# Kernel optimization log

Measured on AMD Instinct MI355X. Metric: run time of the kernel, lower is better.

## Reference

```python
import jax, jax.numpy as jnp
import numpy as np

B, C, KC, H, W = 8, 256, 32, 128, 128


def setup_inputs() -> dict:
    key = jax.random.key(0)
    ks = jax.random.split(key, 5)
    x = jax.random.normal(ks[0], (B, C, H, W), dtype=jnp.float32)
    Wq = jax.random.normal(ks[1], (KC, C), dtype=jnp.float32) / np.sqrt(C)
    Wk = jax.random.normal(ks[2], (KC, C), dtype=jnp.float32) / np.sqrt(C)
    Wv = jax.random.normal(ks[3], (C, C), dtype=jnp.float32) / np.sqrt(C)
    bq = jnp.zeros((KC,), dtype=jnp.float32)
    bk = jnp.zeros((KC,), dtype=jnp.float32)
    bv = jnp.zeros((C,), dtype=jnp.float32)
    gamma = jax.random.uniform(ks[4], (1,), dtype=jnp.float32)
    return {"x": x, "Wq": Wq, "bq": bq, "Wk": Wk, "bk": bk, "Wv": Wv, "bv": bv, "gamma": gamma}


def reference(x, Wq, bq, Wk, bk, Wv, bv, gamma):
    b, c, h, w = x.shape
    n = h * w
    xf = x.reshape(b, c, n)  # [B,C,N]
    # 1x1 convs == per-pixel linear maps
    q = jnp.einsum('kc,bcn->bkn', Wq, xf) + bq[None, :, None]
    k = jnp.einsum('kc,bcn->bkn', Wk, xf) + bk[None, :, None]
    v = jnp.einsum('vc,bcn->bvn', Wv, xf) + bv[None, :, None]
    fm = lambda t: jax.nn.elu(t) + 1.0  # elu+1 feature map
    qm = fm(q)  # [B,KC,N]
    km = fm(k)  # [B,KC,N]
    kv = jnp.einsum('bkn,bvn->bkv', km, v)          # kv context [B,KC,C]
    z = km.sum(axis=-1)                              # z norm factor [B,KC]
    qkv = jnp.einsum('bkn,bkv->bnv', qm, kv)        # [B,N,C]
    qz = jnp.einsum('bkn,bk->bn', qm, z)            # [B,N]
    normed = qkv / jnp.maximum(qz, 1e-6)[..., None]  # [B,N,C]
    out = normed.transpose(0, 2, 1).reshape(b, c, h, w)
    return gamma[0] * out + x
```

## Files before the change

### kernel.cpp

```cpp
#include <hip/hip_runtime.h>

#define Bn  8
#define Cn  256
#define KCn 32
#define Nn  16384

typedef __attribute__((ext_vector_type(8))) short bf16x8;
typedef __attribute__((ext_vector_type(4))) short short4v;
typedef __attribute__((ext_vector_type(4))) float f32x4;

__device__ __forceinline__ float elup1(float v) {
    return v > 0.0f ? v + 1.0f : __expf(v);
}
__device__ __forceinline__ short f2bf(float f) {
    unsigned u = __float_as_uint(f);
    return (short)((u + 0x7FFFu + ((u >> 16) & 1u)) >> 16);
}

__global__ __launch_bounds__(512, 4) void k_km_S(const float* __restrict__ x,
                                                 const float* __restrict__ Wk,
                                                 const float* __restrict__ bk,
                                                 float* __restrict__ S,
                                                 float* __restrict__ Z) {
    __shared__ short xs[256][40];
    __shared__ short wks[32][264];
    __shared__ short kml[32][264];
    __shared__ float bkl[KCn];

    const int t = threadIdx.x;
    const int b = blockIdx.y;
    const int n0 = blockIdx.x * 256;
    const int lane = t & 63, wv = t >> 6;
    const int g = lane >> 4, l15 = lane & 15;
    const int pxw = wv * 32;
    const float* xb = x + (size_t)b * Cn * Nn;

    {
        const int row = t >> 4, col0 = (t & 15) * 16;
        const float* src = Wk + row * Cn + col0;
        bf16x8 v0, v1;
#pragma unroll
        for (int i = 0; i < 8; ++i) { v0[i] = f2bf(src[i]); v1[i] = f2bf(src[8 + i]); }
        *(bf16x8*)&wks[row][col0] = v0;
        *(bf16x8*)&wks[row][col0 + 8] = v1;
        if (t < KCn) bkl[t] = bk[t];
    }

    f32x4 acc1[2][2] = {};
    for (int kc = 0; kc < 8; ++kc) {
        if (kc) __syncthreads();
        {
            const int px = t & 255, ch = t >> 8;
            const float* sp = xb + (size_t)(kc * 32 + ch * 16) * Nn + n0 + px;
            bf16x8 v0, v1;
#pragma unroll
            for (int i = 0; i < 8; ++i) v0[i] = f2bf(sp[(size_t)i * Nn]);
#pragma unroll
            for (int i = 0; i < 8; ++i) v1[i] = f2bf(sp[(size_t)(8 + i) * Nn]);
            *(bf16x8*)&xs[px][ch * 16] = v0;
            *(bf16x8*)&xs[px][ch * 16 + 8] = v1;
        }
        __syncthreads();
        const bf16x8 af0 = *(const bf16x8*)&wks[l15][kc * 32 + g * 8];
        const bf16x8 af1 = *(const bf16x8*)&wks[16 + l15][kc * 32 + g * 8];
        const bf16x8 bf0 = *(const bf16x8*)&xs[pxw + l15][g * 8];
        const bf16x8 bf1 = *(const bf16x8*)&xs[pxw + 16 + l15][g * 8];
        acc1[0][0] = __builtin_amdgcn_mfma_f32_16x16x32_bf16(af0, bf0, acc1[0][0], 0, 0, 0);
        acc1[0][1] = __builtin_amdgcn_mfma_f32_16x16x32_bf16(af0, bf1, acc1[0][1], 0, 0, 0);
        acc1[1][0] = __builtin_amdgcn_mfma_f32_16x16x32_bf16(af1, bf0, acc1[1][0], 0, 0, 0);
        acc1[1][1] = __builtin_amdgcn_mfma_f32_16x16x32_bf16(af1, bf1, acc1[1][1], 0, 0, 0);
    }

    {
        float zp[2][4] = {{0.f,0.f,0.f,0.f},{0.f,0.f,0.f,0.f}};
#pragma unroll
        for (int mt = 0; mt < 2; ++mt)
#pragma unroll
            for (int j = 0; j < 4; ++j) {
                const int kf = mt * 16 + g * 4 + j;
                const float bkv = bkl[kf];
#pragma unroll
                for (int nt = 0; nt < 2; ++nt) {
                    const float v = elup1(acc1[mt][nt][j] + bkv);
                    zp[mt][j] += v;
                    kml[kf][pxw + nt * 16 + l15] = f2bf(v);
                }
            }
#pragma unroll
        for (int mt = 0; mt < 2; ++mt)
#pragma unroll
            for (int j = 0; j < 4; ++j) {
                float s = zp[mt][j];
                s += __shfl_xor(s, 1); s += __shfl_xor(s, 2);
                s += __shfl_xor(s, 4); s += __shfl_xor(s, 8);
                if (l15 == 0) atomicAdd(&Z[b * KCn + mt * 16 + g * 4 + j], s);
            }
    }
    __syncthreads();

    f32x4 acc2[2][2] = {};
    const int crow = wv * 32;
    for (int ks = 0; ks < 8; ++ks) {
        bf16x8 a2[2];
#pragma unroll
        for (int mt = 0; mt < 2; ++mt) {
            const float* ap = xb + (size_t)(crow + mt * 16 + l15) * Nn + n0 + ks * 32 + g * 8;
            const float4 f0 = *(const float4*)ap;
            const float4 f1 = *(const float4*)(ap + 4);
            bf16x8 v;
            v[0] = f2bf(f0.x); v[1] = f2bf(f0.y); v[2] = f2bf(f0.z); v[3] = f2bf(f0.w);
            v[4] = f2bf(f1.x); v[5] = f2bf(f1.y); v[6] = f2bf(f1.z); v[7] = f2bf(f1.w);
            a2[mt] = v;
        }
        const bf16x8 b20 = *(const bf16x8*)&kml[l15][ks * 32 + g * 8];
        const bf16x8 b21 = *(const bf16x8*)&kml[16 + l15][ks * 32 + g * 8];
        acc2[0][0] = __builtin_amdgcn_mfma_f32_16x16x32_bf16(a2[0], b20, acc2[0][0], 0, 0, 0);
        acc2[0][1] = __builtin_amdgcn_mfma_f32_16x16x32_bf16(a2[0], b21, acc2[0][1], 0, 0, 0);
        acc2[1][0] = __builtin_amdgcn_mfma_f32_16x16x32_bf16(a2[1], b20, acc2[1][0], 0, 0, 0);
        acc2[1][1] = __builtin_amdgcn_mfma_f32_16x16x32_bf16(a2[1], b21, acc2[1][1], 0, 0, 0);
    }
    float* Sb = S + (size_t)b * Cn * KCn;
#pragma unroll
    for (int mt = 0; mt < 2; ++mt)
#pragma unroll
        for (int nt = 0; nt < 2; ++nt)
#pragma unroll
            for (int j = 0; j < 4; ++j)
                atomicAdd(&Sb[(crow + mt * 16 + g * 4 + j) * KCn + nt * 16 + l15],
                          acc2[mt][nt][j]);
}

__global__ __launch_bounds__(256) void k_kv(const float* __restrict__ Wv,
                                            const float* __restrict__ bv,
                                            const float* __restrict__ S,
                                            const float* __restrict__ Z,
                                            unsigned short* __restrict__ KVT) {
    __shared__ float Sl[Cn][KCn];
    __shared__ float zl[KCn];
    const int t = threadIdx.x;
    const int b = blockIdx.y;
    const int vc0 = blockIdx.x * 32;
    const float* Sb = S + (size_t)b * Cn * KCn;
#pragma unroll
    for (int i = 0; i < 32; ++i) ((float*)Sl)[i * 256 + t] = Sb[i * 256 + t];
    if (t < KCn) zl[t] = Z[b * KCn + t];
    __syncthreads();
    const int vc = vc0 + (t >> 3);
    const int kq = (t & 7) * 4;
    const float bvv = bv[vc];
    f32x4 acc;
#pragma unroll
    for (int i = 0; i < 4; ++i) acc[i] = bvv * zl[kq + i];
    const float* wv = Wv + (size_t)vc * Cn;
#pragma unroll 4
    for (int c = 0; c < Cn; ++c) {
        const float w = wv[c];
        const f32x4 s4 = *(const f32x4*)&Sl[c][kq];
#pragma unroll
        for (int i = 0; i < 4; ++i) acc[i] += w * s4[i];
    }
    unsigned short* kp = KVT + ((size_t)b * Cn + vc) * KCn + kq;
    ushort4 o;
    o.x = (unsigned short)f2bf(acc[0]); o.y = (unsigned short)f2bf(acc[1]);
    o.z = (unsigned short)f2bf(acc[2]); o.w = (unsigned short)f2bf(acc[3]);
    *(ushort4*)kp = o;
}

__global__ __launch_bounds__(512, 4) void k_out(const float* __restrict__ x,
                                                const float* __restrict__ Wq,
                                                const float* __restrict__ bq,
                                                const unsigned short* __restrict__ KVT,
                                                const float* __restrict__ Z,
                                                const float* __restrict__ gamma,
                                                float* __restrict__ out) {
    __shared__ short xs[256][40];
    __shared__ short wqs[32][264];
    __shared__ short qml[256][40];
    __shared__ short kvtl[272][40];
    __shared__ float bql[KCn];

    const int t = threadIdx.x;
    const int b = blockIdx.y;
    const int n0 = blockIdx.x * 256;
    const int lane = t & 63, wv = t >> 6;
    const int g = lane >> 4, l15 = lane & 15;
    const int pxw = wv * 32;
    const float* xb = x + (size_t)b * Cn * Nn;

    {
        const int row = t >> 4, col0 = (t & 15) * 16;
        const float* src = Wq + row * Cn + col0;
        bf16x8 v0, v1;
#pragma unroll
        for (int i = 0; i < 8; ++i) { v0[i] = f2bf(src[i]); v1[i] = f2bf(src[8 + i]); }
        *(bf16x8*)&wqs[row][col0] = v0;
        *(bf16x8*)&wqs[row][col0 + 8] = v1;
        if (t < KCn) bql[t] = bq[t];
        const int vc = t >> 1, half = t & 1;
        const bf16x8* kvsrc =
            (const bf16x8*)(KVT + (size_t)b * Cn * KCn + vc * KCn + half * 16);
        *(bf16x8*)&kvtl[vc][half * 16]     = kvsrc[0];
        *(bf16x8*)&kvtl[vc][half * 16 + 8] = kvsrc[1];
        if (t < KCn) kvtl[256][t] = f2bf(Z[b * KCn + t]);
        for (int i = t; i < 15 * 40; i += 512) kvtl[257 + i / 40][i % 40] = 0;
    }

    f32x4 acc1[2][2] = {};
    for (int kc = 0; kc < 8; ++kc) {
        if (kc) __syncthreads();
        {
            const int px = t & 255, ch = t >> 8;
            const float* sp = xb + (size_t)(kc * 32 + ch * 16) * Nn + n0 + px;
            bf16x8 v0, v1;
#pragma unroll
            for (int i = 0; i < 8; ++i) v0[i] = f2bf(sp[(size_t)i * Nn]);
#pragma unroll
            for (int i = 0; i < 8; ++i) v1[i] = f2bf(sp[(size_t)(8 + i) * Nn]);
            *(bf16x8*)&xs[px][ch * 16] = v0;
            *(bf16x8*)&xs[px][ch * 16 + 8] = v1;
        }
        __syncthreads();
        const bf16x8 af0 = *(const bf16x8*)&wqs[l15][kc * 32 + g * 8];
        const bf16x8 af1 = *(const bf16x8*)&wqs[16 + l15][kc * 32 + g * 8];
        const bf16x8 bf0 = *(const bf16x8*)&xs[pxw + l15][g * 8];
        const bf16x8 bf1 = *(const bf16x8*)&xs[pxw + 16 + l15][g * 8];
        acc1[0][0] = __builtin_amdgcn_mfma_f32_16x16x32_bf16(af0, bf0, acc1[0][0], 0, 0, 0);
        acc1[0][1] = __builtin_amdgcn_mfma_f32_16x16x32_bf16(af0, bf1, acc1[0][1], 0, 0, 0);
        acc1[1][0] = __builtin_amdgcn_mfma_f32_16x16x32_bf16(af1, bf0, acc1[1][0], 0, 0, 0);
        acc1[1][1] = __builtin_amdgcn_mfma_f32_16x16x32_bf16(af1, bf1, acc1[1][1], 0, 0, 0);
    }

#pragma unroll
    for (int mt = 0; mt < 2; ++mt)
#pragma unroll
        for (int nt = 0; nt < 2; ++nt) {
            short4v q4;
#pragma unroll
            for (int j = 0; j < 4; ++j)
                q4[j] = f2bf(elup1(acc1[mt][nt][j] + bql[mt * 16 + g * 4 + j]));
            *(short4v*)&qml[pxw + nt * 16 + l15][mt * 16 + g * 4] = q4;
        }

    const bf16x8 qb0 = *(const bf16x8*)&qml[pxw + l15][g * 8];
    const bf16x8 qb1 = *(const bf16x8*)&qml[pxw + 16 + l15][g * 8];
    f32x4 u0 = {}, u1 = {};
    {
        const bf16x8 az = *(const bf16x8*)&kvtl[256 + l15][g * 8];
        u0 = __builtin_amdgcn_mfma_f32_16x16x32_bf16(az, qb0, u0, 0, 0, 0);
        u1 = __builtin_amdgcn_mfma_f32_16x16x32_bf16(az, qb1, u1, 0, 0, 0);
    }
    const float qz0 = __shfl(u0[0], l15);
    const float qz1 = __shfl(u1[0], l15);
    const float gm = gamma[0];
    const float r0 = gm / fmaxf(qz0, 1e-6f);
    const float r1 = gm / fmaxf(qz1, 1e-6f);
    float* ob = out + (size_t)b * Cn * Nn + n0;
    const float* xrb = xb + n0;
    const int p0 = pxw + l15, p1 = pxw + 16 + l15;
#pragma unroll 4
    for (int mt = 0; mt < 16; ++mt) {
        const bf16x8 a = *(const bf16x8*)&kvtl[mt * 16 + l15][g * 8];
        f32x4 c0 = {}, c1 = {};
        c0 = __builtin_amdgcn_mfma_f32_16x16x32_bf16(a, qb0, c0, 0, 0, 0);
        c1 = __builtin_amdgcn_mfma_f32_16x16x32_bf16(a, qb1, c1, 0, 0, 0);
#pragma unroll
        for (int j = 0; j < 4; ++j) {
            const size_t ro = (size_t)(mt * 16 + g * 4 + j) * Nn;
            ob[ro + p0] = c0[j] * r0 + xrb[ro + p0];
            ob[ro + p1] = c1[j] * r1 + xrb[ro + p1];
        }
    }
}

extern "C" void kernel_launch(void* const* d_in, const int* in_sizes, int n_in,
                              void* d_out, int out_size, void* d_ws, size_t ws_size,
                              hipStream_t stream) {
    const float* x     = (const float*)d_in[0];
    const float* Wq    = (const float*)d_in[1];
    const float* bq    = (const float*)d_in[2];
    const float* Wk    = (const float*)d_in[3];
    const float* bk    = (const float*)d_in[4];
    const float* Wv    = (const float*)d_in[5];
    const float* bv    = (const float*)d_in[6];
    const float* gamma = (const float*)d_in[7];
    float* out = (float*)d_out;

    float* S = (float*)d_ws;
    float* Z = S + (size_t)Bn * Cn * KCn;
    unsigned short* KVT = (unsigned short*)(Z + (size_t)Bn * KCn);

    hipMemsetAsync(d_ws, 0, ((size_t)Bn * Cn * KCn + Bn * KCn) * sizeof(float), stream);
    k_km_S<<<dim3(64, Bn), 512, 0, stream>>>(x, Wk, bk, S, Z);
    k_kv  <<<dim3(8, Bn), 256, 0, stream>>>(Wv, bv, S, Z, KVT);
    k_out <<<dim3(64, Bn), 512, 0, stream>>>(x, Wq, bq, KVT, Z, gamma, out);
}
```

Before: 394.4 us.

## Halve pixel tile, pre-convert weights to bf16, and register-prefetch x loads

Adds a tiny prep kernel that converts Wk and Wq to bf16 once, so the main kernels stop converting the weights per block into shared memory and read them directly from global. Both heavy kernels now use 128-pixel tiles with twice as many blocks, smaller shared memory footprints and higher occupancy bounds. The x tile for the next channel chunk is prefetched into registers while the current MFMA step runs. k_out reuses the x staging buffer for the q features. The trade-off is an extra launch, double-counted block setup, more Z atomics, and uncached global weight fragment loads per wave.

```diff
diff --git a/kernel.cpp b/kernel.cpp
--- a/kernel.cpp
+++ b/kernel.cpp
@@ -17,90 +17,79 @@
     return (short)((u + 0x7FFFu + ((u >> 16) & 1u)) >> 16);
 }
 
-__global__ __launch_bounds__(512, 4) void k_km_S(const float* __restrict__ x,
-                                                 const float* __restrict__ Wk,
+__global__ void k_prep(const float* __restrict__ Wk, const float* __restrict__ Wq,
+                       unsigned short* __restrict__ Wkbf, unsigned short* __restrict__ Wqbf) {
+    const int i = blockIdx.x * 512 + threadIdx.x;
+    Wkbf[i] = (unsigned short)f2bf(Wk[i]);
+    Wqbf[i] = (unsigned short)f2bf(Wq[i]);
+}
+
+__global__ __launch_bounds__(512, 8) void k_km_S(const float* __restrict__ x,
+                                                 const unsigned short* __restrict__ Wkbf,
                                                  const float* __restrict__ bk,
                                                  float* __restrict__ S,
                                                  float* __restrict__ Z) {
-    __shared__ short xs[256][40];
-    __shared__ short wks[32][264];
-    __shared__ short kml[32][264];
+    __shared__ short xs[128][40];
+    __shared__ short kml[32][136];
     __shared__ float bkl[KCn];
 
-    const int t = threadIdx.x;
-    const int b = blockIdx.y;
-    const int n0 = blockIdx.x * 256;
+    const int t = threadIdx.x, b = blockIdx.y, n0 = blockIdx.x * 128;
     const int lane = t & 63, wv = t >> 6;
     const int g = lane >> 4, l15 = lane & 15;
-    const int pxw = wv * 32;
+    const int pxw = wv * 16;
     const float* xb = x + (size_t)b * Cn * Nn;
-
-    {
-        const int row = t >> 4, col0 = (t & 15) * 16;
-        const float* src = Wk + row * Cn + col0;
-        bf16x8 v0, v1;
-#pragma unroll
-        for (int i = 0; i < 8; ++i) { v0[i] = f2bf(src[i]); v1[i] = f2bf(src[8 + i]); }
-        *(bf16x8*)&wks[row][col0] = v0;
-        *(bf16x8*)&wks[row][col0 + 8] = v1;
-        if (t < KCn) bkl[t] = bk[t];
-    }
-
-    f32x4 acc1[2][2] = {};
+    if (t < KCn) bkl[t] = bk[t];
+
+    const int px = t & 127, ch = t >> 7;
+    const float* xpp = xb + n0 + px;
+    float ld[8];
+#pragma unroll
+    for (int i = 0; i < 8; ++i) ld[i] = xpp[(size_t)(ch * 8 + i) * Nn];
+    const unsigned short* wk0 = Wkbf + l15 * Cn;
+    const unsigned short* wk1 = Wkbf + (16 + l15) * Cn;
+    bf16x8 wa0 = *(const bf16x8*)(wk0);
+    bf16x8 wa1 = *(const bf16x8*)(wk1);
+
+    f32x4 acc1[2] = {};
     for (int kc = 0; kc < 8; ++kc) {
-        if (kc) __syncthreads();
-        {
-            const int px = t & 255, ch = t >> 8;
-            const float* sp = xb + (size_t)(kc * 32 + ch * 16) * Nn + n0 + px;
-            bf16x8 v0, v1;
-#pragma unroll
-            for (int i = 0; i < 8; ++i) v0[i] = f2bf(sp[(size_t)i * Nn]);
-#pragma unroll
-            for (int i = 0; i < 8; ++i) v1[i] = f2bf(sp[(size_t)(8 + i) * Nn]);
-            *(bf16x8*)&xs[px][ch * 16] = v0;
-            *(bf16x8*)&xs[px][ch * 16 + 8] = v1;
-        }
-        __syncthreads();
-        const bf16x8 af0 = *(const bf16x8*)&wks[l15][kc * 32 + g * 8];
-        const bf16x8 af1 = *(const bf16x8*)&wks[16 + l15][kc * 32 + g * 8];
+        __syncthreads();
+        bf16x8 v;
+#pragma unroll
+        for (int i = 0; i < 8; ++i) v[i] = f2bf(ld[i]);
+        *(bf16x8*)&xs[px][ch * 8] = v;
+        __syncthreads();
+        bf16x8 wn0 = wa0, wn1 = wa1;
+        if (kc < 7) {
+            const float* sp = xpp + (size_t)((kc + 1) * 32 + ch * 8) * Nn;
+#pragma unroll
+            for (int i = 0; i < 8; ++i) ld[i] = sp[(size_t)i * Nn];
+            wn0 = *(const bf16x8*)(wk0 + (kc + 1) * 32);
+            wn1 = *(const bf16x8*)(wk1 + (kc + 1) * 32);
+        }
         const bf16x8 bf0 = *(const bf16x8*)&xs[pxw + l15][g * 8];
-        const bf16x8 bf1 = *(const bf16x8*)&xs[pxw + 16 + l15][g * 8];
-        acc1[0][0] = __builtin_amdgcn_mfma_f32_16x16x32_bf16(af0, bf0, acc1[0][0], 0, 0, 0);
-        acc1[0][1] = __builtin_amdgcn_mfma_f32_16x16x32_bf16(af0, bf1, acc1[0][1], 0, 0, 0);
-        acc1[1][0] = __builtin_amdgcn_mfma_f32_16x16x32_bf16(af1, bf0, acc1[1][0], 0, 0, 0);
-        acc1[1][1] = __builtin_amdgcn_mfma_f32_16x16x32_bf16(af1, bf1, acc1[1][1], 0, 0, 0);
-    }
-
-    {
-        float zp[2][4] = {{0.f,0.f,0.f,0.f},{0.f,0.f,0.f,0.f}};
-#pragma unroll
-        for (int mt = 0; mt < 2; ++mt)
-#pragma unroll
-            for (int j = 0; j < 4; ++j) {
-                const int kf = mt * 16 + g * 4 + j;
-                const float bkv = bkl[kf];
-#pragma unroll
-                for (int nt = 0; nt < 2; ++nt) {
-                    const float v = elup1(acc1[mt][nt][j] + bkv);
-                    zp[mt][j] += v;
-                    kml[kf][pxw + nt * 16 + l15] = f2bf(v);
-                }
-            }
-#pragma unroll
-        for (int mt = 0; mt < 2; ++mt)
-#pragma unroll
-            for (int j = 0; j < 4; ++j) {
-                float s = zp[mt][j];
-                s += __shfl_xor(s, 1); s += __shfl_xor(s, 2);
-                s += __shfl_xor(s, 4); s += __shfl_xor(s, 8);
-                if (l15 == 0) atomicAdd(&Z[b * KCn + mt * 16 + g * 4 + j], s);
-            }
-    }
+        acc1[0] = __builtin_amdgcn_mfma_f32_16x16x32_bf16(wa0, bf0, acc1[0], 0, 0, 0);
+        acc1[1] = __builtin_amdgcn_mfma_f32_16x16x32_bf16(wa1, bf0, acc1[1], 0, 0, 0);
+        wa0 = wn0; wa1 = wn1;
+    }
+
+#pragma unroll
+    for (int mt = 0; mt < 2; ++mt)
+#pragma unroll
+        for (int j = 0; j < 4; ++j) {
+            const int kf = mt * 16 + g * 4 + j;
+            const float vv = elup1(acc1[mt][j] + bkl[kf]);
+            kml[kf][pxw + l15] = f2bf(vv);
+            float s = vv;
+            s += __shfl_xor(s, 1); s += __shfl_xor(s, 2);
+            s += __shfl_xor(s, 4); s += __shfl_xor(s, 8);
+            if (l15 == 0) atomicAdd(&Z[b * KCn + kf], s);
+        }
     __syncthreads();
 
     f32x4 acc2[2][2] = {};
     const int crow = wv * 32;
-    for (int ks = 0; ks < 8; ++ks) {
+#pragma unroll
+    for (int ks = 0; ks < 4; ++ks) {
         bf16x8 a2[2];
 #pragma unroll
         for (int mt = 0; mt < 2; ++mt) {
@@ -166,108 +155,95 @@
     *(ushort4*)kp = o;
 }
 
-__global__ __launch_bounds__(512, 4) void k_out(const float* __restrict__ x,
-                                                const float* __restrict__ Wq,
+__global__ __launch_bounds__(512, 8) void k_out(const float* __restrict__ x,
+                                                const unsigned short* __restrict__ Wqbf,
                                                 const float* __restrict__ bq,
                                                 const unsigned short* __restrict__ KVT,
                                                 const float* __restrict__ Z,
                                                 const float* __restrict__ gamma,
                                                 float* __restrict__ out) {
-    __shared__ short xs[256][40];
-    __shared__ short wqs[32][264];
-    __shared__ short qml[256][40];
+    __shared__ short xsu[128 * 40];
     __shared__ short kvtl[272][40];
     __shared__ float bql[KCn];
 
-    const int t = threadIdx.x;
-    const int b = blockIdx.y;
-    const int n0 = blockIdx.x * 256;
+    const int t = threadIdx.x, b = blockIdx.y, n0 = blockIdx.x * 128;
     const int lane = t & 63, wv = t >> 6;
     const int g = lane >> 4, l15 = lane & 15;
-    const int pxw = wv * 32;
+    const int pxw = wv * 16;
     const float* xb = x + (size_t)b * Cn * Nn;
 
     {
-        const int row = t >> 4, col0 = (t & 15) * 16;
-        const float* src = Wq + row * Cn + col0;
-        bf16x8 v0, v1;
-#pragma unroll
-        for (int i = 0; i < 8; ++i) { v0[i] = f2bf(src[i]); v1[i] = f2bf(src[8 + i]); }
-        *(bf16x8*)&wqs[row][col0] = v0;
-        *(bf16x8*)&wqs[row][col0 + 8] = v1;
-        if (t < KCn) bql[t] = bq[t];
         const int vc = t >> 1, half = t & 1;
-        const bf16x8* kvsrc =
-            (const bf16x8*)(KVT + (size_t)b * Cn * KCn + vc * KCn + half * 16);
-        *(bf16x8*)&kvtl[vc][half * 16]     = kvsrc[0];
-        *(bf16x8*)&kvtl[vc][half * 16 + 8] = kvsrc[1];
-        if (t < KCn) kvtl[256][t] = f2bf(Z[b * KCn + t]);
+        const bf16x8* src = (const bf16x8*)(KVT + ((size_t)b * Cn + vc) * KCn + half * 16);
+        *(bf16x8*)&kvtl[vc][half * 16]     = src[0];
+        *(bf16x8*)&kvtl[vc][half * 16 + 8] = src[1];
+        if (t < KCn) { bql[t] = bq[t]; kvtl[256][t] = f2bf(Z[b * KCn + t]); }
         for (int i = t; i < 15 * 40; i += 512) kvtl[257 + i / 40][i % 40] = 0;
     }
 
-    f32x4 acc1[2][2] = {};
+    const int px = t & 127, ch = t >> 7;
+    const float* xpp = xb + n0 + px;
+    float ld[8];
+#pragma unroll
+    for (int i = 0; i < 8; ++i) ld[i] = xpp[(size_t)(ch * 8 + i) * Nn];
+    const unsigned short* wq0 = Wqbf + l15 * Cn;
+    const unsigned short* wq1 = Wqbf + (16 + l15) * Cn;
+    bf16x8 wa0 = *(const bf16x8*)(wq0);
+    bf16x8 wa1 = *(const bf16x8*)(wq1);
+
+    short (*xs)[40] = (short(*)[40])xsu;
+    f32x4 acc1[2] = {};
     for (int kc = 0; kc < 8; ++kc) {
-        if (kc) __syncthreads();
-        {
-            const int px = t & 255, ch = t >> 8;
-            const float* sp = xb + (size_t)(kc * 32 + ch * 16) * Nn + n0 + px;
-            bf16x8 v0, v1;
-#pragma unroll
-            for (int i = 0; i < 8; ++i) v0[i] = f2bf(sp[(size_t)i * Nn]);
-#pragma unroll
-            for (int i = 0; i < 8; ++i) v1[i] = f2bf(sp[(size_t)(8 + i) * Nn]);
-            *(bf16x8*)&xs[px][ch * 16] = v0;
-            *(bf16x8*)&xs[px][ch * 16 + 8] = v1;
-        }
-        __syncthreads();
-        const bf16x8 af0 = *(const bf16x8*)&wqs[l15][kc * 32 + g * 8];
-        const bf16x8 af1 = *(const bf16x8*)&wqs[16 + l15][kc * 32 + g * 8];
+        __syncthreads();
+        bf16x8 v;
+#pragma unroll
+        for (int i = 0; i < 8; ++i) v[i] = f2bf(ld[i]);
+        *(bf16x8*)&xs[px][ch * 8] = v;
+        __syncthreads();
+        bf16x8 wn0 = wa0, wn1 = wa1;
+        if (kc < 7) {
+            const float* sp = xpp + (size_t)((kc + 1) * 32 + ch * 8) * Nn;
+#pragma unroll
+            for (int i = 0; i < 8; ++i) ld[i] = sp[(size_t)i * Nn];
+            wn0 = *(const bf16x8*)(wq0 + (kc + 1) * 32);
+            wn1 = *(const bf16x8*)(wq1 + (kc + 1) * 32);
+        }
         const bf16x8 bf0 = *(const bf16x8*)&xs[pxw + l15][g * 8];
-        const bf16x8 bf1 = *(const bf16x8*)&xs[pxw + 16 + l15][g * 8];
-        acc1[0][0] = __builtin_amdgcn_mfma_f32_16x16x32_bf16(af0, bf0, acc1[0][0], 0, 0, 0);
-        acc1[0][1] = __builtin_amdgcn_mfma_f32_16x16x32_bf16(af0, bf1, acc1[0][1], 0, 0, 0);
-        acc1[1][0] = __builtin_amdgcn_mfma_f32_16x16x32_bf16(af1, bf0, acc1[1][0], 0, 0, 0);
-        acc1[1][1] = __builtin_amdgcn_mfma_f32_16x16x32_bf16(af1, bf1, acc1[1][1], 0, 0, 0);
-    }
-
-#pragma unroll
-    for (int mt = 0; mt < 2; ++mt)
-#pragma unroll
-        for (int nt = 0; nt < 2; ++nt) {
-            short4v q4;
-#pragma unroll
-            for (int j = 0; j < 4; ++j)
-                q4[j] = f2bf(elup1(acc1[mt][nt][j] + bql[mt * 16 + g * 4 + j]));
-            *(short4v*)&qml[pxw + nt * 16 + l15][mt * 16 + g * 4] = q4;
-        }
-
-    const bf16x8 qb0 = *(const bf16x8*)&qml[pxw + l15][g * 8];
-    const bf16x8 qb1 = *(const bf16x8*)&qml[pxw + 16 + l15][g * 8];
-    f32x4 u0 = {}, u1 = {};
+        acc1[0] = __builtin_amdgcn_mfma_f32_16x16x32_bf16(wa0, bf0, acc1[0], 0, 0, 0);
+        acc1[1] = __builtin_amdgcn_mfma_f32_16x16x32_bf16(wa1, bf0, acc1[1], 0, 0, 0);
+        wa0 = wn0; wa1 = wn1;
+    }
+    __syncthreads();
+
+    short* qml = xsu;
+#pragma unroll
+    for (int mt = 0; mt < 2; ++mt) {
+        short4v q4;
+#pragma unroll
+        for (int j = 0; j < 4; ++j)
+            q4[j] = f2bf(elup1(acc1[mt][j] + bql[mt * 16 + g * 4 + j]));
+        *(short4v*)&qml[(pxw + l15) * 32 + mt * 16 + g * 4] = q4;
+    }
+
+    const bf16x8 qb0 = *(const bf16x8*)&qml[(pxw + l15) * 32 + g * 8];
+    f32x4 u0 = {};
     {
         const bf16x8 az = *(const bf16x8*)&kvtl[256 + l15][g * 8];
         u0 = __builtin_amdgcn_mfma_f32_16x16x32_bf16(az, qb0, u0, 0, 0, 0);
-        u1 = __builtin_amdgcn_mfma_f32_16x16x32_bf16(az, qb1, u1, 0, 0, 0);
-    }
-    const float qz0 = __shfl(u0[0], l15);
-    const float qz1 = __shfl(u1[0], l15);
-    const float gm = gamma[0];
-    const float r0 = gm / fmaxf(qz0, 1e-6f);
-    const float r1 = gm / fmaxf(qz1, 1e-6f);
-    float* ob = out + (size_t)b * Cn * Nn + n0;
-    const float* xrb = xb + n0;
-    const int p0 = pxw + l15, p1 = pxw + 16 + l15;
+    }
+    const float qz = __shfl(u0[0], l15);
+    const float r = gamma[0] / fmaxf(qz, 1e-6f);
+    const float* xr = xb + n0 + pxw + l15;
+    float* ob = out + (size_t)b * Cn * Nn + n0 + pxw + l15;
 #pragma unroll 4
     for (int mt = 0; mt < 16; ++mt) {
         const bf16x8 a = *(const bf16x8*)&kvtl[mt * 16 + l15][g * 8];
-        f32x4 c0 = {}, c1 = {};
+        f32x4 c0 = {};
         c0 = __builtin_amdgcn_mfma_f32_16x16x32_bf16(a, qb0, c0, 0, 0, 0);
-        c1 = __builtin_amdgcn_mfma_f32_16x16x32_bf16(a, qb1, c1, 0, 0, 0);
 #pragma unroll
         for (int j = 0; j < 4; ++j) {
             const size_t ro = (size_t)(mt * 16 + g * 4 + j) * Nn;
-            ob[ro + p0] = c0[j] * r0 + xrb[ro + p0];
-            ob[ro + p1] = c1[j] * r1 + xrb[ro + p1];
+            ob[ro] = c0[j] * r + xr[ro];
         }
     }
 }
@@ -287,10 +263,13 @@
 
     float* S = (float*)d_ws;
     float* Z = S + (size_t)Bn * Cn * KCn;
-    unsigned short* KVT = (unsigned short*)(Z + (size_t)Bn * KCn);
+    unsigned short* KVT  = (unsigned short*)(Z + (size_t)Bn * KCn);
+    unsigned short* Wkbf = KVT + (size_t)Bn * Cn * KCn;
+    unsigned short* Wqbf = Wkbf + (size_t)KCn * Cn;
 
     hipMemsetAsync(d_ws, 0, ((size_t)Bn * Cn * KCn + Bn * KCn) * sizeof(float), stream);
-    k_km_S<<<dim3(64, Bn), 512, 0, stream>>>(x, Wk, bk, S, Z);
+    k_prep<<<dim3(16), 512, 0, stream>>>(Wk, Wq, Wkbf, Wqbf);
+    k_km_S<<<dim3(128, Bn), 512, 0, stream>>>(x, Wkbf, bk, S, Z);
     k_kv  <<<dim3(8, Bn), 256, 0, stream>>>(Wv, bv, S, Z, KVT);
-    k_out <<<dim3(64, Bn), 512, 0, stream>>>(x, Wq, bq, KVT, Z, gamma, out);
-}
+    k_out <<<dim3(128, Bn), 512, 0, stream>>>(x, Wqbf, bq, KVT, Z, gamma, out);
+}
```

Result: slower. 546.6 us (+38.6%).
